# Kernel optimization log

Hardware: AMD Instinct MI355X
Metric: run time of the kernel (lower is better)

The kernel has to match this reference:

```python
import jax, jax.numpy as jnp
import numpy as np

K = 75        # kpoints
L = 8         # number of labels (output_dim)


def _knn_nonconformity(q, t, train_label, k=K, num_labels=L):
    """Brute-force kNN (Euclidean) + distance-weighted nonconformity.
    q: [B, D] queries; t: [N, D] train bank; train_label: [N] int.
    Returns [B, num_labels]: for each class i, sum of 1/dist over the k
    nearest neighbors whose label != i (0 weight for zero distance)."""
    # squared distances [B, N]
    d2 = (jnp.sum(q * q, axis=1, keepdims=True)
          - 2.0 * q @ t.T
          + jnp.sum(t * t, axis=1)[None, :])
    d2 = jnp.maximum(d2, 0.0)
    neg_top, idx = jax.lax.top_k(-d2, k)          # k smallest d2
    dist = jnp.sqrt(jnp.maximum(-neg_top, 0.0))    # [B, k]
    safe = jnp.where(dist > 0, dist, 1.0)
    w = jnp.where(dist > 0, 1.0 / safe, 0.0)       # [B, k]
    mismatch = 1.0 - jax.nn.one_hot(train_label[idx], num_labels, dtype=w.dtype)  # [B,k,L]
    return jnp.einsum('bk,bkl->bl', w, mismatch)


def setup_inputs() -> dict:
    key = jax.random.key(0)
    ks = jax.random.split(key, 12)
    B, N, D, H, C = 1024, 50000, 83, 128, 10000
    s = lambda fan_in: 1.0 / np.sqrt(fan_in)
    return {
        'x': jax.random.normal(ks[0], (B, D), jnp.float32),
        'train_x': jax.random.normal(ks[1], (N, D), jnp.float32),
        'train_label': jax.random.randint(ks[2], (N,), 0, L, jnp.int32),
        'cali': jax.random.uniform(ks[3], (C,), jnp.float32) * 50.0,
        'W1': jax.random.normal(ks[4], (D, H), jnp.float32) * s(D),
        'b1': jnp.zeros((H,), jnp.float32),
        'W2': jax.random.normal(ks[5], (H, H), jnp.float32) * s(H),
        'b2': jnp.zeros((H,), jnp.float32),
        'W3': jax.random.normal(ks[6], (H, H), jnp.float32) * s(H),
        'b3': jnp.zeros((H,), jnp.float32),
        'W4': jax.random.normal(ks[7], (H, L), jnp.float32) * s(H),
        'b4': jnp.zeros((L,), jnp.float32),
    }


def reference(x, train_x, train_label, cali, W1, b1, W2, b2, W3, b3, W4, b4):
    relu = jax.nn.relu
    # query-side MLP (inference: dropout inactive)
    h1 = relu(x @ W1 + b1)
    h2 = relu(h1 @ W2 + b2)
    h3 = relu(h2 @ W3 + b3)
    out = jax.nn.softmax(h3 @ W4 + b4, axis=-1)
    # train-side feature banks (what each kNTree was fit on)
    t1 = relu(train_x @ W1 + b1)
    t2 = relu(t1 @ W2 + b2)
    t3 = relu(t2 @ W3 + b3)
    t4 = jax.nn.softmax(t3 @ W4 + b4, axis=-1)
    # per-layer nonconformity [B, L], summed across the 5 layers
    total = (_knn_nonconformity(x, train_x, train_label)
             + _knn_nonconformity(h1, t1, train_label)
             + _knn_nonconformity(h2, t2, train_label)
             + _knn_nonconformity(h3, t3, train_label)
             + _knn_nonconformity(out, t4, train_label))
    # empirical p-value: fraction of calibration scores >= total nonconformity
    counts = jnp.sum(cali[None, None, :] >= total[:, :, None], axis=-1)  # [B, L]
    return counts.astype(jnp.float32) / cali.shape[0]
```

## Files before the change

### kernel.cpp

```cpp
#include <hip/hip_runtime.h>
#include <math.h>

#define KNN 75
#define NL 8
#define NB 1024
#define NT 50000
#define NT_PAD 50048
#define NCALI 10000
#define KC 32
#define TT 128
#define NTB 391
#define SLOTS 16
#define CAP 6144
#define NSUB 2048
#define NSB 16
#define SSTRIDE 24
#define SOFF 11
#define RSEL 32

typedef __attribute__((ext_vector_type(8))) short bf16x8;
typedef __attribute__((ext_vector_type(4))) float f32x4;

__device__ __forceinline__ int swz(int c){ return c + ((c>>5)<<2); }

__device__ __forceinline__ unsigned short f2bf_rn(float x){
  unsigned u = __float_as_uint(x);
  unsigned r = (u + 0x7FFFu + ((u>>16)&1u)) >> 16;
  return (unsigned short)r;
}
__device__ __forceinline__ float bf2f(unsigned short h){
  return __uint_as_float(((unsigned)h)<<16);
}
__device__ __forceinline__ bf16x8 ld8(const unsigned short* p){
  return *(const bf16x8*)p;
}
__device__ __forceinline__ void gl_lds16(const unsigned short* g, unsigned short* l){
  __builtin_amdgcn_global_load_lds(
      (const __attribute__((address_space(1))) void*)g,
      (__attribute__((address_space(3))) void*)l, 16, 0, 0);
}

__global__ void pad_copy_k(const float* __restrict__ in, float* __restrict__ out,
                           int M, int Din, int Dout){
  int idx = blockIdx.x*256 + threadIdx.x;
  if (idx >= M*Dout) return;
  int r = idx / Dout, c = idx - r*Dout;
  out[idx] = (c < Din) ? in[r*Din + c] : 0.f;
}

__global__ void wsplit_k(const float* __restrict__ W, int kreal, int dp,
                         unsigned short* __restrict__ WtH,
                         unsigned short* __restrict__ WtL){
  int idx = blockIdx.x*256 + threadIdx.x;
  if (idx >= 128*dp) return;
  int n = idx / dp, k = idx - n*dp;
  float v = (k < kreal) ? W[(size_t)k*128 + n] : 0.f;
  unsigned short h = f2bf_rn(v);
  WtH[idx] = h;
  WtL[idx] = f2bf_rn(v - bf2f(h));
}

__global__ __launch_bounds__(256) void mlp_gemm_k(
    const float* __restrict__ A, int lda, int kchunks,
    const float* __restrict__ W, int kreal,
    const float* __restrict__ bias,
    float* __restrict__ Out, int M)
{
  __shared__ float As[KC][132];
  __shared__ float Bs[KC][148];
  int tid = threadIdx.x;
  int r0 = (tid>>4)*8, c0 = (tid&15)*8;
  int rowBase = blockIdx.x*128;
  float acc[8][8];
  #pragma unroll
  for (int i=0;i<8;i++)
    #pragma unroll
    for (int j=0;j<8;j++) acc[i][j]=0.f;

  for (int kc=0;kc<kchunks;kc++){
    { int rr = tid>>3, k4=(tid&7)*4;
      #pragma unroll
      for (int i=0;i<4;i++){
        int row = rr + i*32, gr = rowBase + row;
        float4 v = make_float4(0.f,0.f,0.f,0.f);
        if (gr < M) v = *(const float4*)&A[(size_t)gr*lda + kc*KC + k4];
        As[k4+0][row]=v.x; As[k4+1][row]=v.y; As[k4+2][row]=v.z; As[k4+3][row]=v.w;
      }
    }
    { int kk=tid>>5, c4=(tid&31)*4;
      #pragma unroll
      for (int i=0;i<4;i++){
        int k = kk + i*8, gk = kc*KC + k;
        float4 v = make_float4(0.f,0.f,0.f,0.f);
        if (gk < kreal) v = *(const float4*)&W[(size_t)gk*128 + c4];
        *(float4*)&Bs[k][swz(c4)] = v;
      }
    }
    __syncthreads();
    #pragma unroll 4
    for (int k=0;k<KC;k++){
      float4 a0 = *(const float4*)&As[k][r0];
      float4 a1 = *(const float4*)&As[k][r0+4];
      float4 b0 = *(const float4*)&Bs[k][swz(c0)];
      float4 b1 = *(const float4*)&Bs[k][swz(c0+4)];
      float av[8] = {a0.x,a0.y,a0.z,a0.w,a1.x,a1.y,a1.z,a1.w};
      float bv[8] = {b0.x,b0.y,b0.z,b0.w,b1.x,b1.y,b1.z,b1.w};
      #pragma unroll
      for (int i=0;i<8;i++)
        #pragma unroll
        for (int j=0;j<8;j++) acc[i][j] += av[i]*bv[j];
    }
    __syncthreads();
  }
  float bb[8];
  #pragma unroll
  for (int j=0;j<8;j++) bb[j]=bias[c0+j];
  #pragma unroll
  for (int i=0;i<8;i++){
    int gr = rowBase + r0 + i;
    if (gr < M){
      float o[8];
      #pragma unroll
      for (int j=0;j<8;j++){ float v=acc[i][j]+bb[j]; o[j]=v>0.f?v:0.f; }
      *(float4*)&Out[(size_t)gr*128 + c0]   = make_float4(o[0],o[1],o[2],o[3]);
      *(float4*)&Out[(size_t)gr*128 + c0+4] = make_float4(o[4],o[5],o[6],o[7]);
    }
  }
}

__global__ void mlp8_k(const float* __restrict__ A, const float* __restrict__ W4,
                       const float* __restrict__ b4, float* __restrict__ Out, int M){
  __shared__ float Ws[128*8];
  int tid = threadIdx.x;
  for (int i=tid;i<1024;i+=256) Ws[i]=W4[i];
  __syncthreads();
  int r = blockIdx.x*32 + (tid>>3), c = tid&7;
  if (r >= M) return;
  const float* a = &A[(size_t)r*128];
  float acc = b4[c];
  #pragma unroll 16
  for (int k=0;k<128;k++) acc += a[k]*Ws[k*8+c];
  Out[(size_t)r*32 + c] = acc;
}

__global__ void softmax_k(float* __restrict__ X, int M){
  int r = blockIdx.x*256 + threadIdx.x;
  if (r >= M) return;
  float* p = &X[(size_t)r*32];
  float v[8], m=-1e30f;
  #pragma unroll
  for (int j=0;j<8;j++){ v[j]=p[j]; m = v[j]>m ? v[j] : m; }
  float s=0.f;
  #pragma unroll
  for (int j=0;j<8;j++){ v[j]=__expf(v[j]-m); s+=v[j]; }
  float inv=1.f/s;
  #pragma unroll
  for (int j=0;j<8;j++) p[j]=v[j]*inv;
  #pragma unroll
  for (int j=8;j<32;j++) p[j]=0.f;
}

__global__ void conv_norm_k(
    const float* __restrict__ XA, unsigned short* __restrict__ HA,
    unsigned short* __restrict__ LA, float* __restrict__ nA, int MA,
    const float* __restrict__ XB, unsigned short* __restrict__ HB,
    unsigned short* __restrict__ LB, float* __restrict__ nB, int MB,
    int dp)
{
  int w = threadIdx.x>>6, lane = threadIdx.x&63;
  int row = blockIdx.x*4 + w;
  const float* src; unsigned short* dh; unsigned short* dl; float* nrm;
  if (row < MA){
    src=&XA[(size_t)row*dp]; dh=&HA[(size_t)row*dp]; dl=&LA[(size_t)row*dp]; nrm=&nA[row];
  } else {
    int r2 = row - MA;
    if (r2 >= MB) return;
    src=&XB[(size_t)r2*dp]; dh=&HB[(size_t)r2*dp]; dl=&LB[(size_t)r2*dp]; nrm=&nB[r2];
  }
  float s=0.f;
  for (int c=lane*2; c<dp; c+=128){
    float2 v = *(const float2*)&src[c];
    s += v.x*v.x + v.y*v.y;
    unsigned short h0 = f2bf_rn(v.x), h1 = f2bf_rn(v.y);
    float r0 = v.x - bf2f(h0), r1 = v.y - bf2f(h1);
    ushort2 hh; hh.x=h0; hh.y=h1;
    ushort2 ll; ll.x=f2bf_rn(r0); ll.y=f2bf_rn(r1);
    *(ushort2*)&dh[c]=hh;
    *(ushort2*)&dl[c]=ll;
  }
  #pragma unroll
  for (int off=32;off>0;off>>=1) s += __shfl_down(s, off, 64);
  if (lane==0) *nrm=s;
}

__device__ __forceinline__ void find_bin(int* hist, int* part, int nb, int Krem,
                                         int tid, int* s_B, int* s_lob){
  int ch = nb>>8;
  int base = tid*ch;
  int s=0;
  for (int b=base;b<base+ch;b++) s+=hist[b];
  int lane = tid & 63, wv = tid>>6;
  int v = s;
  #pragma unroll
  for (int off=1; off<64; off<<=1){
    int u = __shfl_up(v, off, 64);
    if (lane >= off) v += u;
  }
  if (lane==63) part[wv] = v;
  __syncthreads();
  int wbase = 0;
  #pragma unroll
  for (int w2=0; w2<4; w2++) wbase += (w2 < wv) ? part[w2] : 0;
  v += wbase;
  int excl = v - s;
  if (v >= Krem && excl < Krem){
    int lob = excl, B = base + ch - 1;
    for (int b=base;b<base+ch;b++){
      if (lob + hist[b] >= Krem){ B=b; break; }
      lob += hist[b];
    }
    *s_B = B; *s_lob = lob;
  }
  if (tid==255 && v < Krem){ *s_B = nb-1; *s_lob = 0; }
  __syncthreads();
}

__global__ __launch_bounds__(256) void sel64_k(const unsigned* __restrict__ skeys,
                                               unsigned* __restrict__ Tthr){
  __shared__ unsigned buf[NSUB];
  __shared__ int hist[2048];
  __shared__ int part[256];
  __shared__ int sB, sLob;
  int tid=threadIdx.x, q=blockIdx.x;
  for (int i=tid;i<NSUB;i+=256) buf[i]=skeys[(size_t)q*NSUB+i];
  int Krem=RSEL;
  for (int i=tid;i<2048;i+=256) hist[i]=0;
  __syncthreads();
  for (int i=tid;i<NSUB;i+=256) atomicAdd(&hist[buf[i]>>21],1);
  __syncthreads();
  find_bin(hist,part,2048,Krem,tid,&sB,&sLob);
  unsigned pre=(unsigned)sB; Krem-=sLob;
  for (int i=tid;i<2048;i+=256) hist[i]=0;
  __syncthreads();
  for (int i=tid;i<NSUB;i+=256){ unsigned k=buf[i]; if ((k>>21)==pre) atomicAdd(&hist[(k>>10)&0x7FFu],1); }
  __syncthreads();
  find_bin(hist,part,2048,Krem,tid,&sB,&sLob);
  pre=(pre<<11)|(unsigned)sB; Krem-=sLob;
  for (int i=tid;i<1024;i+=256) hist[i]=0;
  __syncthreads();
  for (int i=tid;i<NSUB;i+=256){ unsigned k=buf[i]; if ((k>>10)==pre) atomicAdd(&hist[k&0x3FFu],1); }
  __syncthreads();
  find_bin(hist,part,1024,Krem,tid,&sB,&sLob);
  if (tid==0) Tthr[q]=(pre<<10)|(unsigned)sB;
}

#define MFMA_SEC(BHC, BLC, AH, AL)                                               \
  _Pragma("unroll")                                                              \
  for (int tj=0;tj<8;tj++){                                                      \
    int rowB = tj*16 + col;                                                      \
    int sw = (((quad + (rowB>>1)) & 3) << 3);                                    \
    bf16x8 bh = *(const bf16x8*)&(BHC)[rowB*32 + sw];                            \
    bf16x8 bl = *(const bf16x8*)&(BLC)[rowB*32 + sw];                            \
    acc[tj] = __builtin_amdgcn_mfma_f32_16x16x32_bf16(AH, bh, acc[tj], 0,0,0);   \
    acc[tj] = __builtin_amdgcn_mfma_f32_16x16x32_bf16(AH, bl, acc[tj], 0,0,0);   \
    acc[tj] = __builtin_amdgcn_mfma_f32_16x16x32_bf16(AL, bh, acc[tj], 0,0,0);   \
  }

#define MFMA_KLOOP(ROWMAP)                                                       \
  size_t aoff = (size_t)(qbase + w*16 + col)*dp + quad*8;                        \
  const unsigned short* pAH = QH + aoff;                                         \
  const unsigned short* pAL = QL + aoff;                                         \
  int i0 = tid,      row0 = i0>>2, sg0 = ((i0&3) - (row0>>1)) & 3;               \
  int i1 = tid+256,  row1 = i1>>2, sg1 = ((i1&3) - (row1>>1)) & 3;               \
  size_t g0 = (size_t)(ROWMAP(n0+row0))*dp + (size_t)sg0*8;                      \
  size_t g1 = (size_t)(ROWMAP(n0+row1))*dp + (size_t)sg1*8;                      \
  f32x4 acc[8];                                                                  \
  _Pragma("unroll")                                                              \
  for (int tj=0;tj<8;tj++){ f32x4 z={0.f,0.f,0.f,0.f}; acc[tj]=z; }              \
  gl_lds16(TH + g0, BH0 + i0*8);                                                 \
  gl_lds16(TH + g1, BH0 + i1*8);                                                 \
  gl_lds16(TL + g0, BL0 + i0*8);                                                 \
  gl_lds16(TL + g1, BL0 + i1*8);                                                 \
  bf16x8 xh = ld8(pAH), xl = ld8(pAL);                                           \
  bf16x8 yh = xh, yl = xl;                                                       \
  _Pragma("unroll")                                                              \
  for (int kc=0; kc<kchunks; kc+=2){                                             \
    __syncthreads();                                                             \
    if (kc+1 < kchunks){                                                         \
      size_t ko=(size_t)(kc+1)*32;                                               \
      gl_lds16(TH + g0 + ko, BH1 + i0*8);                                        \
      gl_lds16(TH + g1 + ko, BH1 + i1*8);                                        \
      gl_lds16(TL + g0 + ko, BL1 + i0*8);                                        \
      gl_lds16(TL + g1 + ko, BL1 + i1*8);                                        \
      yh = ld8(pAH + ko); yl = ld8(pAL + ko);                                    \
    }                                                                            \
    MFMA_SEC(BH0, BL0, xh, xl);                                                  \
    if (kc+1 < kchunks){                                                         \
      __syncthreads();                                                           \
      if (kc+2 < kchunks){                                                       \
        size_t ko=(size_t)(kc+2)*32;                                             \
        gl_lds16(TH + g0 + ko, BH0 + i0*8);                                      \
        gl_lds16(TH + g1 + ko, BH0 + i1*8);                                      \
        gl_lds16(TL + g0 + ko, BL0 + i0*8);                                      \
        gl_lds16(TL + g1 + ko, BL0 + i1*8);                                      \
        xh = ld8(pAH + ko); xl = ld8(pAL + ko);                                  \
      }                                                                          \
      MFMA_SEC(BH1, BL1, yh, yl);                                                \
    }                                                                            \
  }

#define ROW_ID(r) (r)
#define ROW_SUB(r) ((r)*SSTRIDE + SOFF)

template<int KCH>
__global__ __launch_bounds__(256) void dist_mfma_k(
    const unsigned short* __restrict__ QH, const unsigned short* __restrict__ QL,
    const unsigned short* __restrict__ TH, const unsigned short* __restrict__ TL,
    const float* __restrict__ qn, const float* __restrict__ tn,
    const int* __restrict__ labels, const unsigned* __restrict__ Tthr,
    unsigned* __restrict__ slab)
{
  constexpr int dp = KCH*32;
  __shared__ __align__(16) unsigned short smem[4*4096];
  unsigned short* BH0 = smem;
  unsigned short* BH1 = smem + 4096;
  unsigned short* BL0 = smem + 8192;
  unsigned short* BL1 = smem + 12288;
  unsigned (*hitbuf)[SLOTS] = (unsigned (*)[SLOTS])smem;
  int* hcnt = (int*)(smem + 4096);
  int b = blockIdx.x;
  int xcd = b & 7, s = b >> 3;
  int qb = s & 15, tslot = s >> 4;
  int t_blk = xcd + 8*tslot;
  if (t_blk >= NTB) return;
  int tid = threadIdx.x, w = tid>>6, lane = tid&63;
  int quad = lane>>4, col = lane&15;
  int qbase = qb*64;
  int n0 = t_blk*TT;
  constexpr int kchunks = KCH;

  MFMA_KLOOP(ROW_ID)

  __syncthreads();
  if (tid<64) hcnt[tid]=0;
  __syncthreads();
  float qnr[4]; unsigned Tq[4]; float thrF[4];
  #pragma unroll
  for (int r=0;r<4;r++){
    int q = qbase + w*16 + quad*4 + r;
    qnr[r]  = qn[q];
    Tq[r]   = Tthr[q];
    thrF[r] = __uint_as_float(Tq[r] | 7u);
  }
  #pragma unroll
  for (int tj=0;tj<8;tj++){
    int t = n0 + tj*16 + col;
    if (t < NT){
      float tnv = tn[t];
      unsigned lab = (unsigned)labels[t];
      #pragma unroll
      for (int r=0;r<4;r++){
        float d2 = fmaf(-2.f, acc[tj][r], qnr[r] + tnv);
        if (d2 <= thrF[r]){
          float d2c = fmaxf(d2, 0.f);
          unsigned key = (__float_as_uint(d2c)&0xFFFFFFF8u) | lab;
          if (key < Tq[r]){
            int ql = w*16 + quad*4 + r;
            int idx = atomicAdd(&hcnt[ql], 1);
            if (idx < SLOTS-1) hitbuf[ql][1+idx] = key;
          }
        }
      }
    }
  }
  __syncthreads();
  if (tid<64) hitbuf[tid][0]=(unsigned)hcnt[tid];
  __syncthreads();
  {
    int q = tid>>2, sub = (tid&3)*4;
    uint4 v = *(uint4*)&hitbuf[q][sub];
    *(uint4*)&slab[((size_t)(qbase+q)*NTB + t_blk)*SLOTS + sub] = v;
  }
}

template<int KCH>
__global__ __launch_bounds__(256) void dist_sub_k(
    const unsigned short* __restrict__ QH, const unsigned short* __restrict__ QL,
    const unsigned short* __restrict__ TH, const unsigned short* __restrict__ TL,
    const float* __restrict__ qn, const float* __restrict__ tn,
    const int* __restrict__ labels, unsigned* __restrict__ keys)
{
  constexpr int dp = KCH*32;
  __shared__ __align__(16) unsigned short smem[4*4096];
  unsigned short* BH0 = smem;
  unsigned short* BH1 = smem + 4096;
  unsigned short* BL0 = smem + 8192;
  unsigned short* BL1 = smem + 12288;
  int b = blockIdx.x;
  int qb = b & 15, t_blk = b >> 4;
  int tid = threadIdx.x, w = tid>>6, lane = tid&63;
  int quad = lane>>4, col = lane&15;
  int qbase = qb*64;
  int n0 = t_blk*TT;
  constexpr int kchunks = KCH;

  MFMA_KLOOP(ROW_SUB)

  float qnr[4];
  #pragma unroll
  for (int r=0;r<4;r++)
    qnr[r] = qn[qbase + w*16 + quad*4 + r];
  #pragma unroll
  for (int tj=0;tj<8;tj++){
    int sI = n0 + tj*16 + col;
    int g  = sI*SSTRIDE + SOFF;
    float tnv = tn[g];
    unsigned lab = (unsigned)labels[g];
    #pragma unroll
    for (int r=0;r<4;r++){
      float d2 = fmaxf(fmaf(-2.f, acc[tj][r], qnr[r] + tnv), 0.f);
      unsigned key = (__float_as_uint(d2)&0xFFFFFFF8u) | lab;
      int q = qbase + w*16 + quad*4 + r;
      keys[(size_t)q*NSUB + sI] = key;
    }
  }
}

template<int KCH>
__global__ __launch_bounds__(256) void mlp_mfma_k(
    const unsigned short* __restrict__ QH, const unsigned short* __restrict__ QL,
    const unsigned short* __restrict__ TH, const unsigned short* __restrict__ TL,
    const float* __restrict__ bias, float* __restrict__ Out, int M)
{
  constexpr int dp = KCH*32;
  __shared__ __align__(16) unsigned short smem[4*4096];
  unsigned short* BH0 = smem;
  unsigned short* BH1 = smem + 4096;
  unsigned short* BL0 = smem + 8192;
  unsigned short* BL1 = smem + 12288;
  int tid = threadIdx.x, w = tid>>6, lane = tid&63;
  int quad = lane>>4, col = lane&15;
  int qbase = blockIdx.x*64;
  int n0 = 0;
  constexpr int kchunks = KCH;

  MFMA_KLOOP(ROW_ID)

  float bb[8];
  #pragma unroll
  for (int tj=0;tj<8;tj++) bb[tj] = bias[tj*16 + col];
  #pragma unroll
  for (int r=0;r<4;r++){
    int row = qbase + w*16 + quad*4 + r;
    if (row < M){
      #pragma unroll
      for (int tj=0;tj<8;tj++){
        float v = acc[tj][r] + bb[tj];
        Out[(size_t)row*128 + tj*16 + col] = v > 0.f ? v : 0.f;
      }
    }
  }
}

__global__ __launch_bounds__(256) void final_k(
    const unsigned* __restrict__ slab,
    const float* __restrict__ Qm, const float* __restrict__ Tm,
    const float* __restrict__ qn, const float* __restrict__ tn,
    const int* __restrict__ labels,
    float* __restrict__ tot, int first, int dp)
{
  __shared__ int hist[2048];
  __shared__ int part[256];
  __shared__ unsigned buf[CAP];
  __shared__ unsigned lowbuf[96];
  __shared__ float qrow[128];
  __shared__ int sB,sLob,s_cnt,s_low,s_bad;
  __shared__ float s_w[9];
  int tid=threadIdx.x, q=blockIdx.x;
  if (tid==0){ for (int j=0;j<9;j++) s_w[j]=0.f; s_cnt=0; s_low=0; s_bad=0; }
  __syncthreads();

  const unsigned* sq = slab + (size_t)q*NTB*SLOTS;
  for (int sidx=tid; sidx<NTB; sidx+=256){
    const unsigned* s = sq + (size_t)sidx*SLOTS;
    uint4 a = *(const uint4*)s;
    unsigned cnt = a.x;
    if (cnt > SLOTS-1){ s_bad=1; continue; }
    if (!cnt) continue;
    int base = atomicAdd(&s_cnt, (int)cnt);
    if (base + (int)cnt <= CAP){
      buf[base] = a.y;
      if (cnt>=2) buf[base+1] = a.z;
      if (cnt>=3) buf[base+2] = a.w;
      for (unsigned w=4; w<=cnt; w++) buf[base+w-1] = s[w];
    }
  }
  __syncthreads();
  int total = s_cnt;
  int bad = s_bad;

#define CONTRIB(kk) do{ float d2_=__uint_as_float((kk)&0xFFFFFFF8u); \
    if (d2_>0.f){ float w_=1.0f/sqrtf(d2_); \
      atomicAdd(&s_w[8],w_); atomicAdd(&s_w[(kk)&7u],w_); } }while(0)

  unsigned T; int Krem=KNN;
  if (!bad && total>=KNN && total<=CAP){
    for (int i=tid;i<2048;i+=256) hist[i]=0;
    __syncthreads();
    for (int i=tid;i<total;i+=256) atomicAdd(&hist[buf[i]>>21],1);
    __syncthreads();
    find_bin(hist,part,2048,Krem,tid,&sB,&sLob);
    unsigned pre=(unsigned)sB; Krem-=sLob;
    for (int i=tid;i<2048;i+=256) hist[i]=0;
    __syncthreads();
    for (int i=tid;i<total;i+=256){ unsigned k=buf[i]; if ((k>>21)==pre) atomicAdd(&hist[(k>>10)&0x7FFu],1); }
    __syncthreads();
    find_bin(hist,part,2048,Krem,tid,&sB,&sLob);
    pre=(pre<<11)|(unsigned)sB; Krem-=sLob;
    for (int i=tid;i<1024;i+=256) hist[i]=0;
    __syncthreads();
    for (int i=tid;i<total;i+=256){ unsigned k=buf[i]; if ((k>>10)==pre) atomicAdd(&hist[k&0x3FFu],1); }
    __syncthreads();
    find_bin(hist,part,1024,Krem,tid,&sB,&sLob);
    T=(pre<<10)|(unsigned)sB; Krem-=sLob;
    __syncthreads();
    for (int i=tid;i<total;i+=256){ unsigned k=buf[i]; if (k<T) CONTRIB(k); }
  } else {
    if (tid==0) s_cnt=0;
    for (int i=tid;i<dp;i+=256) qrow[i]=Qm[(size_t)q*dp+i];
    __syncthreads();
    float qq=qn[q];
    auto KEY=[&](int t)->unsigned{
      const float* br=&Tm[(size_t)t*dp];
      float dot=0.f;
      for (int k2=0;k2<dp;k2++) dot+=qrow[k2]*br[k2];
      float d2=fmaxf(qq-2.f*dot+tn[t],0.f);
      return (__float_as_uint(d2)&0xFFFFFFF8u)|(unsigned)labels[t];
    };
    for (int i=tid;i<2048;i+=256) hist[i]=0;
    __syncthreads();
    for (int t=tid;t<NT;t+=256) atomicAdd(&hist[KEY(t)>>21],1);
    __syncthreads();
    find_bin(hist,part,2048,Krem,tid,&sB,&sLob);
    int c=hist[sB]; Krem-=sLob;
    unsigned prefix=(unsigned)sB; int shift=21;
    if (c > CAP){
      __syncthreads();
      for (int i=tid;i<2048;i+=256) hist[i]=0;
      __syncthreads();
      for (int t=tid;t<NT;t+=256){ unsigned k=KEY(t); if ((k>>21)==prefix) atomicAdd(&hist[(k>>10)&0x7FFu],1); }
      __syncthreads();
      find_bin(hist,part,2048,Krem,tid,&sB,&sLob);
      c=hist[sB]; Krem-=sLob; prefix=(prefix<<11)|(unsigned)sB; shift=10;
    }
    if (c > CAP){
      __syncthreads();
      for (int i=tid;i<1024;i+=256) hist[i]=0;
      __syncthreads();
      for (int t=tid;t<NT;t+=256){ unsigned k=KEY(t); if ((k>>10)==prefix) atomicAdd(&hist[k&0x3FFu],1); }
      __syncthreads();
      find_bin(hist,part,1024,Krem,tid,&sB,&sLob);
      c=hist[sB]; Krem-=sLob; prefix=(prefix<<10)|(unsigned)sB; shift=0;
    }
    if (c <= CAP){
      for (int t=tid;t<NT;t+=256){
        unsigned k=KEY(t); unsigned pp=k>>shift;
        if (pp==prefix){ int j=atomicAdd(&s_cnt,1); if (j<CAP) buf[j]=k; }
        else if (pp<prefix){ int j=atomicAdd(&s_low,1); if (j<96) lowbuf[j]=k; }
      }
      __syncthreads();
      int sh=shift;
      while (sh>0){
        int nsh=(sh==21)?10:0;
        int nb=1<<(sh-nsh);
        __syncthreads();
        for (int i=tid;i<nb;i+=256) hist[i]=0;
        __syncthreads();
        int cc=s_cnt;
        for (int i=tid;i<cc;i+=256) atomicAdd(&hist[(buf[i]>>nsh)&(unsigned)(nb-1)],1);
        __syncthreads();
        find_bin(hist,part,nb,Krem,tid,&sB,&sLob);
        Krem-=sLob; prefix=(prefix<<(sh-nsh))|(unsigned)sB; sh=nsh;
      }
      T=prefix;
      __syncthreads();
      int lowc=s_low, cc=s_cnt;
      for (int i=tid;i<lowc;i+=256){ unsigned k=lowbuf[i]; CONTRIB(k); }
      for (int i=tid;i<cc;i+=256){ unsigned k=buf[i]; if (k<T) CONTRIB(k); }
    } else {
      T=prefix;
      for (int t=tid;t<NT;t+=256){ unsigned k=KEY(t); if (k<T) CONTRIB(k); }
    }
  }
  __syncthreads();
  if (tid==0){
    float d2=__uint_as_float(T&0xFFFFFFF8u);
    float w=(d2>0.f)?(1.0f/sqrtf(d2)):0.f;
    s_w[8] += (float)Krem*w;
    s_w[T&7u] += (float)Krem*w;
  }
  __syncthreads();
  if (tid<8){
    float contrib = s_w[8]-s_w[tid];
    size_t o=(size_t)q*NL+tid;
    tot[o] = first ? contrib : tot[o]+contrib;
  }
#undef CONTRIB
}

__global__ void pvalue_k(const float* __restrict__ tot, const float* __restrict__ cali,
                         float* __restrict__ out){
  __shared__ float t8[NL];
  __shared__ int part[4][NL];
  int tid=threadIdx.x, q=blockIdx.x;
  if (tid<NL) t8[tid]=tot[(size_t)q*NL+tid];
  __syncthreads();
  float th[NL];
  #pragma unroll
  for (int c=0;c<NL;c++) th[c]=t8[c];
  int cnt[NL];
  #pragma unroll
  for (int c=0;c<NL;c++) cnt[c]=0;
  for (int i=tid;i<NCALI;i+=256){
    float v=cali[i];
    #pragma unroll
    for (int c=0;c<NL;c++) cnt[c] += (v>=th[c]) ? 1 : 0;
  }
  #pragma unroll
  for (int c=0;c<NL;c++){
    #pragma unroll
    for (int off=32;off>0;off>>=1) cnt[c]+=__shfl_down(cnt[c],off,64);
  }
  if ((tid&63)==0){
    #pragma unroll
    for (int c=0;c<NL;c++) part[tid>>6][c]=cnt[c];
  }
  __syncthreads();
  if (tid<NL){
    int s=part[0][tid]+part[1][tid]+part[2][tid]+part[3][tid];
    out[(size_t)q*NL+tid] = (float)s / 10000.f;
  }
}

template<int KCH>
static void knn_layer(const float* Qm, const float* Bank, float* qnl, int first,
                      const int* lbl, float* tnb,
                      unsigned short* qH, unsigned short* qL,
                      unsigned short* bankH, unsigned short* bankL,
                      unsigned* skeys, unsigned* sT, unsigned* slab,
                      float* tot, hipStream_t stream){
  constexpr int dp = KCH*32;
  conv_norm_k<<<(NT+NB)/4,256,0,stream>>>(Bank, bankH, bankL, tnb, NT,
                                          Qm, qH, qL, qnl, NB, dp);
  dist_sub_k<KCH><<<16*NSB,256,0,stream>>>(qH,qL,bankH,bankL,qnl,tnb,lbl,skeys);
  sel64_k<<<NB,256,0,stream>>>(skeys,sT);
  dist_mfma_k<KCH><<<8*16*49,256,0,stream>>>(qH,qL,bankH,bankL,qnl,tnb,lbl,sT,slab);
  final_k<<<NB,256,0,stream>>>(slab,Qm,Bank,qnl,tnb,lbl,tot,first,dp);
}

extern "C" void kernel_launch(void* const* d_in, const int* in_sizes, int n_in,
                              void* d_out, int out_size, void* d_ws, size_t ws_size,
                              hipStream_t stream) {
  const float* x   = (const float*)d_in[0];
  const float* txr = (const float*)d_in[1];
  const int*   lbl = (const int*)  d_in[2];
  const float* cal = (const float*)d_in[3];
  const float* W1  = (const float*)d_in[4];
  const float* b1  = (const float*)d_in[5];
  const float* W2  = (const float*)d_in[6];
  const float* b2  = (const float*)d_in[7];
  const float* W3  = (const float*)d_in[8];
  const float* b3  = (const float*)d_in[9];
  const float* W4  = (const float*)d_in[10];
  const float* b4  = (const float*)d_in[11];
  float* out = (float*)d_out;
  float* ws  = (float*)d_ws;

  size_t off=0;
  float* xq0=ws+off; off+=(size_t)NB*96;
  float* xq1=ws+off; off+=(size_t)NB*128;
  float* xq2=ws+off; off+=(size_t)NB*128;
  float* xq3=ws+off; off+=(size_t)NB*128;
  float* xq4=ws+off; off+=(size_t)NB*32;
  float* tbA=ws+off; off+=(size_t)NT*128;
  float* tbB=ws+off; off+=(size_t)NT*128;
  float* tb4=ws+off; off+=(size_t)NT*32;
  float* qnb=ws+off; off+=(size_t)5*NB;
  float* tnb=ws+off; off+=(size_t)NT;
  float* tot=ws+off; off+=(size_t)NB*NL;
  unsigned* sT=(unsigned*)(ws+off); off+=NB;
  unsigned short* qH=(unsigned short*)(ws+off); off+=(size_t)NB*64;
  unsigned short* qL=(unsigned short*)(ws+off); off+=(size_t)NB*64;
  unsigned short* bankH=(unsigned short*)(ws+off); off+=(size_t)NT_PAD*64;
  unsigned short* bankL=(unsigned short*)(ws+off); off+=(size_t)NT_PAD*64;
  unsigned short* wt1H=(unsigned short*)(ws+off); off+=(size_t)128*48;
  unsigned short* wt1L=(unsigned short*)(ws+off); off+=(size_t)128*48;
  unsigned short* wt2H=(unsigned short*)(ws+off); off+=(size_t)128*64;
  unsigned short* wt2L=(unsigned short*)(ws+off); off+=(size_t)128*64;
  unsigned short* wt3H=(unsigned short*)(ws+off); off+=(size_t)128*64;
  unsigned short* wt3L=(unsigned short*)(ws+off); off+=(size_t)128*64;
  off=(off+3)&~(size_t)3;
  unsigned* slab=(unsigned*)(ws+off);
  unsigned* skeys=(unsigned*)(ws+off);
  { size_t slab_sz=(size_t)NB*NTB*SLOTS, skey_sz=(size_t)NB*NSUB;
    off += (slab_sz > skey_sz ? slab_sz : skey_sz); }

  pad_copy_k<<<(NB*96+255)/256,256,0,stream>>>(x, xq0, NB, 83, 96);
  pad_copy_k<<<((size_t)NT*96+255)/256,256,0,stream>>>(txr, tbA, NT, 83, 96);
  wsplit_k<<<(128*96+255)/256,256,0,stream>>>(W1, 83, 96, wt1H, wt1L);
  wsplit_k<<<(128*128+255)/256,256,0,stream>>>(W2, 128, 128, wt2H, wt2L);
  wsplit_k<<<(128*128+255)/256,256,0,stream>>>(W3, 128, 128, wt3H, wt3L);
  mlp_gemm_k<<<(NB+127)/128,256,0,stream>>>(xq0,96,3,W1,83,b1,xq1,NB);
  mlp_gemm_k<<<(NB+127)/128,256,0,stream>>>(xq1,128,4,W2,128,b2,xq2,NB);
  mlp_gemm_k<<<(NB+127)/128,256,0,stream>>>(xq2,128,4,W3,128,b3,xq3,NB);
  mlp8_k<<<(NB+31)/32,256,0,stream>>>(xq3,W4,b4,xq4,NB);
  softmax_k<<<(NB+255)/256,256,0,stream>>>(xq4,NB);

  knn_layer<3>(xq0, tbA, qnb+0*NB, 1, lbl, tnb, qH,qL,bankH,bankL, skeys,sT,slab, tot, stream);
  mlp_mfma_k<3><<<2*NTB,256,0,stream>>>(bankH,bankL,wt1H,wt1L,b1,tbB,NT);
  knn_layer<4>(xq1, tbB, qnb+1*NB, 0, lbl, tnb, qH,qL,bankH,bankL, skeys,sT,slab, tot, stream);
  mlp_mfma_k<4><<<2*NTB,256,0,stream>>>(bankH,bankL,wt2H,wt2L,b2,tbA,NT);
  knn_layer<4>(xq2, tbA, qnb+2*NB, 0, lbl, tnb, qH,qL,bankH,bankL, skeys,sT,slab, tot, stream);
  mlp_mfma_k<4><<<2*NTB,256,0,stream>>>(bankH,bankL,wt3H,wt3L,b3,tbB,NT);
  knn_layer<4>(xq3, tbB, qnb+3*NB, 0, lbl, tnb, qH,qL,bankH,bankL, skeys,sT,slab, tot, stream);
  mlp8_k<<<(NT+31)/32,256,0,stream>>>(tbB,W4,b4,tb4,NT);
  softmax_k<<<(NT+255)/256,256,0,stream>>>(tb4,NT);
  knn_layer<1>(xq4, tb4, qnb+4*NB, 0, lbl, tnb, qH,qL,bankH,bankL, skeys,sT,slab, tot, stream);

  pvalue_k<<<NB,256,0,stream>>>(tot,cal,out);
}
```

Baseline: 760.2 us.

## Fuse prep kernels, query MLP chain, and bank softmax into fewer launches

```diff
diff --git a/kernel.cpp b/kernel.cpp
--- a/kernel.cpp
+++ b/kernel.cpp
@@ -18,6 +18,12 @@
 #define SOFF 11
 #define RSEL 32
 
+#define PB_Q    384
+#define PB_BANK 18750
+#define PB_W1   48
+#define PB_W23  64
+#define PREP_BLOCKS (PB_Q+PB_BANK+PB_W1+2*PB_W23)
+
 typedef __attribute__((ext_vector_type(8))) short bf16x8;
 typedef __attribute__((ext_vector_type(4))) float f32x4;
 
@@ -40,37 +46,49 @@
       (__attribute__((address_space(3))) void*)l, 16, 0, 0);
 }
 
-__global__ void pad_copy_k(const float* __restrict__ in, float* __restrict__ out,
-                           int M, int Din, int Dout){
-  int idx = blockIdx.x*256 + threadIdx.x;
+__device__ __forceinline__ void pad_one(const float* __restrict__ in,
+                                        float* __restrict__ out, int M,
+                                        int Din, int Dout, int idx){
   if (idx >= M*Dout) return;
   int r = idx / Dout, c = idx - r*Dout;
   out[idx] = (c < Din) ? in[r*Din + c] : 0.f;
 }
-
-__global__ void wsplit_k(const float* __restrict__ W, int kreal, int dp,
-                         unsigned short* __restrict__ WtH,
-                         unsigned short* __restrict__ WtL){
-  int idx = blockIdx.x*256 + threadIdx.x;
-  if (idx >= 128*dp) return;
+__device__ __forceinline__ void wsplit_one(const float* __restrict__ W, int kreal,
+                                           int dp, unsigned short* __restrict__ WtH,
+                                           unsigned short* __restrict__ WtL, int idx){
   int n = idx / dp, k = idx - n*dp;
   float v = (k < kreal) ? W[(size_t)k*128 + n] : 0.f;
   unsigned short h = f2bf_rn(v);
   WtH[idx] = h;
   WtL[idx] = f2bf_rn(v - bf2f(h));
 }
-
-__global__ __launch_bounds__(256) void mlp_gemm_k(
-    const float* __restrict__ A, int lda, int kchunks,
-    const float* __restrict__ W, int kreal,
-    const float* __restrict__ bias,
-    float* __restrict__ Out, int M)
+__global__ void prep_k(const float* __restrict__ x, float* __restrict__ xq0,
+                       const float* __restrict__ txr, float* __restrict__ tbA,
+                       const float* __restrict__ W1, unsigned short* wt1H, unsigned short* wt1L,
+                       const float* __restrict__ W2, unsigned short* wt2H, unsigned short* wt2L,
+                       const float* __restrict__ W3, unsigned short* wt3H, unsigned short* wt3L){
+  int b = blockIdx.x, tid = threadIdx.x;
+  if (b < PB_Q){
+    pad_one(x, xq0, NB, 83, 96, b*256 + tid);
+  } else if (b < PB_Q + PB_BANK){
+    pad_one(txr, tbA, NT, 83, 96, (b-PB_Q)*256 + tid);
+  } else if (b < PB_Q + PB_BANK + PB_W1){
+    wsplit_one(W1, 83, 96,  wt1H, wt1L, (b-PB_Q-PB_BANK)*256 + tid);
+  } else if (b < PB_Q + PB_BANK + PB_W1 + PB_W23){
+    wsplit_one(W2, 128, 128, wt2H, wt2L, (b-PB_Q-PB_BANK-PB_W1)*256 + tid);
+  } else {
+    wsplit_one(W3, 128, 128, wt3H, wt3L, (b-PB_Q-PB_BANK-PB_W1-PB_W23)*256 + tid);
+  }
+}
+
+__device__ __forceinline__ void qmlp_layer(
+    const float* __restrict__ srcG, int lda,
+    float (*H)[132], float (*As)[132], float (*Bs)[148],
+    int kchunks, int kreal,
+    const float* __restrict__ W, const float* __restrict__ bias,
+    float* __restrict__ OutG, int rowBase, int tid)
 {
-  __shared__ float As[KC][132];
-  __shared__ float Bs[KC][148];
-  int tid = threadIdx.x;
   int r0 = (tid>>4)*8, c0 = (tid&15)*8;
-  int rowBase = blockIdx.x*128;
   float acc[8][8];
   #pragma unroll
   for (int i=0;i<8;i++)
@@ -81,9 +99,10 @@
     { int rr = tid>>3, k4=(tid&7)*4;
       #pragma unroll
       for (int i=0;i<4;i++){
-        int row = rr + i*32, gr = rowBase + row;
-        float4 v = make_float4(0.f,0.f,0.f,0.f);
-        if (gr < M) v = *(const float4*)&A[(size_t)gr*lda + kc*KC + k4];
+        int row = rr + i*32;
+        float4 v;
+        if (srcG) v = *(const float4*)&srcG[(size_t)(rowBase+row)*lda + kc*KC + k4];
+        else      v = *(const float4*)&H[row][kc*KC + k4];
         As[k4+0][row]=v.x; As[k4+1][row]=v.y; As[k4+2][row]=v.z; As[k4+3][row]=v.w;
       }
     }
@@ -117,19 +136,67 @@
   for (int j=0;j<8;j++) bb[j]=bias[c0+j];
   #pragma unroll
   for (int i=0;i<8;i++){
-    int gr = rowBase + r0 + i;
-    if (gr < M){
-      float o[8];
+    int row = r0 + i;
+    float o[8];
+    #pragma unroll
+    for (int j=0;j<8;j++){ float v=acc[i][j]+bb[j]; o[j]=v>0.f?v:0.f; }
+    *(float4*)&H[row][c0]   = make_float4(o[0],o[1],o[2],o[3]);
+    *(float4*)&H[row][c0+4] = make_float4(o[4],o[5],o[6],o[7]);
+    *(float4*)&OutG[(size_t)(rowBase+row)*128 + c0]   = make_float4(o[0],o[1],o[2],o[3]);
+    *(float4*)&OutG[(size_t)(rowBase+row)*128 + c0+4] = make_float4(o[4],o[5],o[6],o[7]);
+  }
+  __syncthreads();
+}
+
+__global__ __launch_bounds__(256) void qmlp_k(
+    const float* __restrict__ xq0,
+    const float* __restrict__ W1, const float* __restrict__ b1,
+    const float* __restrict__ W2, const float* __restrict__ b2,
+    const float* __restrict__ W3, const float* __restrict__ b3,
+    const float* __restrict__ W4, const float* __restrict__ b4,
+    float* __restrict__ xq1, float* __restrict__ xq2, float* __restrict__ xq3,
+    float* __restrict__ xq4)
+{
+  __shared__ float As[KC][132];
+  __shared__ float Bs[KC][148];
+  __shared__ float H[128][132];
+  int tid = threadIdx.x;
+  int rowBase = blockIdx.x*128;
+
+  qmlp_layer(xq0, 96, H, As, Bs, 3, 83,  W1, b1, xq1, rowBase, tid);
+  qmlp_layer(nullptr, 0, H, As, Bs, 4, 128, W2, b2, xq2, rowBase, tid);
+  qmlp_layer(nullptr, 0, H, As, Bs, 4, 128, W3, b3, xq3, rowBase, tid);
+
+  float* W4s = (float*)Bs;
+  for (int i=tid;i<1024;i+=256) W4s[i]=W4[i];
+  __syncthreads();
+  if (tid < 128){
+    int row = rowBase + tid;
+    float v[8];
+    #pragma unroll
+    for (int c=0;c<8;c++) v[c]=b4[c];
+    for (int k=0;k<128;k++){
+      float a = H[tid][k];
       #pragma unroll
-      for (int j=0;j<8;j++){ float v=acc[i][j]+bb[j]; o[j]=v>0.f?v:0.f; }
-      *(float4*)&Out[(size_t)gr*128 + c0]   = make_float4(o[0],o[1],o[2],o[3]);
-      *(float4*)&Out[(size_t)gr*128 + c0+4] = make_float4(o[4],o[5],o[6],o[7]);
-    }
-  }
-}
-
-__global__ void mlp8_k(const float* __restrict__ A, const float* __restrict__ W4,
-                       const float* __restrict__ b4, float* __restrict__ Out, int M){
+      for (int c=0;c<8;c++) v[c] += a*W4s[k*8+c];
+    }
+    float m=-1e30f;
+    #pragma unroll
+    for (int c=0;c<8;c++) m = v[c]>m ? v[c] : m;
+    float s=0.f;
+    #pragma unroll
+    for (int c=0;c<8;c++){ v[c]=__expf(v[c]-m); s+=v[c]; }
+    float inv=1.f/s;
+    float* p = &xq4[(size_t)row*32];
+    #pragma unroll
+    for (int c=0;c<8;c++) p[c]=v[c]*inv;
+    #pragma unroll
+    for (int j=8;j<32;j++) p[j]=0.f;
+  }
+}
+
+__global__ void mlp8sm_k(const float* __restrict__ A, const float* __restrict__ W4,
+                         const float* __restrict__ b4, float* __restrict__ Out, int M){
   __shared__ float Ws[128*8];
   int tid = threadIdx.x;
   for (int i=tid;i<1024;i+=256) Ws[i]=W4[i];
@@ -140,24 +207,22 @@
   float acc = b4[c];
   #pragma unroll 16
   for (int k=0;k<128;k++) acc += a[k]*Ws[k*8+c];
-  Out[(size_t)r*32 + c] = acc;
-}
-
-__global__ void softmax_k(float* __restrict__ X, int M){
-  int r = blockIdx.x*256 + threadIdx.x;
-  if (r >= M) return;
-  float* p = &X[(size_t)r*32];
-  float v[8], m=-1e30f;
-  #pragma unroll
-  for (int j=0;j<8;j++){ v[j]=p[j]; m = v[j]>m ? v[j] : m; }
+  int lane = tid & 63, base = lane & ~7;
+  float v[8];
+  #pragma unroll
+  for (int j=0;j<8;j++) v[j] = __shfl(acc, base+j, 64);
+  float m=-1e30f;
+  #pragma unroll
+  for (int j=0;j<8;j++) m = v[j]>m ? v[j] : m;
   float s=0.f;
   #pragma unroll
   for (int j=0;j<8;j++){ v[j]=__expf(v[j]-m); s+=v[j]; }
   float inv=1.f/s;
-  #pragma unroll
-  for (int j=0;j<8;j++) p[j]=v[j]*inv;
-  #pragma unroll
-  for (int j=8;j<32;j++) p[j]=0.f;
+  float* p = &Out[(size_t)r*32];
+  p[c]    = v[c]*inv;
+  p[8+c]  = 0.f;
+  p[16+c] = 0.f;
+  p[24+c] = 0.f;
 }
 
 __global__ void conv_norm_k(
@@ -304,7 +369,7 @@
         gl_lds16(TL + g0 + ko, BL0 + i0*8);                                      \
         gl_lds16(TL + g1 + ko, BL0 + i1*8);                                      \
         xh = ld8(pAH + ko); xl = ld8(pAL + ko);                                  \
-      }                                                                          \
+      }                                                                            \
       MFMA_SEC(BH1, BL1, yh, yl);                                                \
     }                                                                            \
   }
@@ -705,16 +770,9 @@
   { size_t slab_sz=(size_t)NB*NTB*SLOTS, skey_sz=(size_t)NB*NSUB;
     off += (slab_sz > skey_sz ? slab_sz : skey_sz); }
 
-  pad_copy_k<<<(NB*96+255)/256,256,0,stream>>>(x, xq0, NB, 83, 96);
-  pad_copy_k<<<((size_t)NT*96+255)/256,256,0,stream>>>(txr, tbA, NT, 83, 96);
-  wsplit_k<<<(128*96+255)/256,256,0,stream>>>(W1, 83, 96, wt1H, wt1L);
-  wsplit_k<<<(128*128+255)/256,256,0,stream>>>(W2, 128, 128, wt2H, wt2L);
-  wsplit_k<<<(128*128+255)/256,256,0,stream>>>(W3, 128, 128, wt3H, wt3L);
-  mlp_gemm_k<<<(NB+127)/128,256,0,stream>>>(xq0,96,3,W1,83,b1,xq1,NB);
-  mlp_gemm_k<<<(NB+127)/128,256,0,stream>>>(xq1,128,4,W2,128,b2,xq2,NB);
-  mlp_gemm_k<<<(NB+127)/128,256,0,stream>>>(xq2,128,4,W3,128,b3,xq3,NB);
-  mlp8_k<<<(NB+31)/32,256,0,stream>>>(xq3,W4,b4,xq4,NB);
-  softmax_k<<<(NB+255)/256,256,0,stream>>>(xq4,NB);
+  prep_k<<<PREP_BLOCKS,256,0,stream>>>(x,xq0,txr,tbA,
+                                       W1,wt1H,wt1L,W2,wt2H,wt2L,W3,wt3H,wt3L);
+  qmlp_k<<<8,256,0,stream>>>(xq0,W1,b1,W2,b2,W3,b3,W4,b4,xq1,xq2,xq3,xq4);
 
   knn_layer<3>(xq0, tbA, qnb+0*NB, 1, lbl, tnb, qH,qL,bankH,bankL, skeys,sT,slab, tot, stream);
   mlp_mfma_k<3><<<2*NTB,256,0,stream>>>(bankH,bankL,wt1H,wt1L,b1,tbB,NT);
@@ -723,8 +781,7 @@
   knn_layer<4>(xq2, tbA, qnb+2*NB, 0, lbl, tnb, qH,qL,bankH,bankL, skeys,sT,slab, tot, stream);
   mlp_mfma_k<4><<<2*NTB,256,0,stream>>>(bankH,bankL,wt3H,wt3L,b3,tbB,NT);
   knn_layer<4>(xq3, tbB, qnb+3*NB, 0, lbl, tnb, qH,qL,bankH,bankL, skeys,sT,slab, tot, stream);
-  mlp8_k<<<(NT+31)/32,256,0,stream>>>(tbB,W4,b4,tb4,NT);
-  softmax_k<<<(NT+255)/256,256,0,stream>>>(tb4,NT);
+  mlp8sm_k<<<(NT+31)/32,256,0,stream>>>(tbB,W4,b4,tb4,NT);
   knn_layer<1>(xq4, tb4, qnb+4*NB, 0, lbl, tnb, qH,qL,bankH,bankL, skeys,sT,slab, tot, stream);
 
   pvalue_k<<<NB,256,0,stream>>>(tot,cal,out);
```

After: 727.7 us. 1.04x faster.
